# Kernel tuning notes

Measured on AMD Instinct MI355X. Metric: run time of the kernel, lower is better.

## Reference

```python
import jax, jax.numpy as jnp
import numpy as np

NUM_HEADS = 16
HEAD_DIM = 64
LN_EPS = 1e-5


def setup_inputs() -> dict:
    key = jax.random.key(0)
    k1, k2, k3, k4 = jax.random.split(key, 4)
    B, N, D = 4, 2048, NUM_HEADS * HEAD_DIM
    q = jax.random.normal(k1, (B, N, D), dtype=jnp.float32)
    k = jax.random.normal(k2, (B, N, D), dtype=jnp.float32)
    v = jax.random.normal(k3, (B, N, D), dtype=jnp.float32)
    W_out = jax.random.normal(k4, (D, D), dtype=jnp.float32) * (1.0 / np.sqrt(D))
    g = jnp.ones((D,), dtype=jnp.float32)
    return {"q": q, "k": k, "v": v, "W_out": W_out, "g": g}


def _split_heads(x):
    b, n, _ = x.shape
    return x.reshape(b, n, NUM_HEADS, HEAD_DIM).transpose(0, 2, 1, 3)  # b h n d


def reference(q, k, v, W_out, g):
    scale = HEAD_DIM ** -0.5
    qh = _split_heads(q) * scale          # [b,h,n,d]
    kh = _split_heads(k)                  # [b,h,m,d]
    vh = _split_heads(v)                  # [b,h,m,d]
    sim = jnp.einsum('bhnd,bhmd->bhnm', qh, kh)
    attn = jax.nn.softmax(sim.astype(jnp.float32), axis=-1)
    out = jnp.einsum('bhnm,bhmd->bhnd', attn, vh)
    b, h, n, d = out.shape
    out = out.transpose(0, 2, 1, 3).reshape(b, n, h * d)  # b n (h d)
    out = out @ W_out.T                   # Linear, no bias
    # LayerNorm (bias=False), biased variance
    mean = jnp.mean(out, axis=-1, keepdims=True)
    var = jnp.var(out, axis=-1, keepdims=True)
    return (out - mean) * jax.lax.rsqrt(var + LN_EPS) * g
```

## Files before the change

kernel.cpp:

```cpp
#include <hip/hip_runtime.h>
#include <hip/hip_bf16.h>


#define Bv 4
#define Nv 2048
#define Hv 16
#define DHv 64
#define Dv 1024
#define NT (Nv / 64)

#define KCONV_BLOCKS 4096
#define WCONV_BLOCKS 512
#define VT_BLOCKS 2048

#define L2E 1.44269504088896340736f

typedef __attribute__((ext_vector_type(8))) short short8;
typedef __attribute__((ext_vector_type(4))) float floatx4;

__device__ inline unsigned pack_bf2(float a, float b) {
    unsigned ua = __builtin_bit_cast(unsigned, a) + 0x8000u;
    unsigned ub = __builtin_bit_cast(unsigned, b) + 0x8000u;
    return __builtin_amdgcn_perm(ub, ua, 0x07060302u);
}

__device__ inline unsigned cvt_pk_bf16(float a, float b) {
    unsigned d;
    asm("v_cvt_pk_bf16_f32 %0, %1, %2" : "=v"(d) : "v"(a), "v"(b));
    return d;
}

__device__ inline unsigned bf2u_rte(float a, float b) {
    unsigned short ua = __builtin_bit_cast(unsigned short, __float2bfloat16(a));
    unsigned short ub = __builtin_bit_cast(unsigned short, __float2bfloat16(b));
    return (unsigned)ua | ((unsigned)ub << 16);
}

__device__ inline float max3f(float a, float b, float c) {
    return fmaxf(fmaxf(a, b), c);
}

__device__ inline void plswap16(unsigned &a, unsigned &b) {
    auto r = __builtin_amdgcn_permlane16_swap(a, b, false, false);
    a = r[0]; b = r[1];
}
__device__ inline void plswap32(unsigned &a, unsigned &b) {
    auto r = __builtin_amdgcn_permlane32_swap(a, b, false, false);
    a = r[0]; b = r[1];
}

__device__ inline float redq_max(float x) {
    unsigned a = __builtin_bit_cast(unsigned, x), b = a;
    plswap16(a, b);
    float m = fmaxf(__builtin_bit_cast(float, a), __builtin_bit_cast(float, b));
    unsigned c = __builtin_bit_cast(unsigned, m), d = c;
    plswap32(c, d);
    return fmaxf(__builtin_bit_cast(float, c), __builtin_bit_cast(float, d));
}

__global__ __launch_bounds__(256)
void prep_all(const float* __restrict__ K, __hip_bfloat16* __restrict__ Kb,
              const float* __restrict__ W, __hip_bfloat16* __restrict__ Wb,
              const float* __restrict__ v, __hip_bfloat16* __restrict__ vt) {
    __shared__ short T[64][76];
    int bid = blockIdx.x;
    if (bid < KCONV_BLOCKS + WCONV_BLOCKS) {
        const float* src;
        __hip_bfloat16* dst;
        if (bid < KCONV_BLOCKS) { src = K; dst = Kb; }
        else { src = W; dst = Wb; bid -= KCONV_BLOCKS; }
        int base = (bid * 256 + threadIdx.x) * 8;
        float4 f0 = *(const float4*)(src + base);
        float4 f1 = *(const float4*)(src + base + 4);
        uint4 u;
        u.x = pack_bf2(f0.x, f0.y);
        u.y = pack_bf2(f0.z, f0.w);
        u.z = pack_bf2(f1.x, f1.y);
        u.w = pack_bf2(f1.z, f1.w);
        *(uint4*)(dst + base) = u;
        return;
    }
    bid -= KCONV_BLOCKS + WCONV_BLOCKS;
    const int b = bid >> 9;
    const int rem = bid & 511;
    const int h = rem >> 5;
    const int n0 = (rem & 31) * 64;
    const int t = threadIdx.x;
    const int ir = t >> 4;
    const int d4 = (t & 15) * 4;
#pragma unroll
    for (int pass = 0; pass < 4; ++pass) {
        int n = pass * 16 + ir;
        float4 f = *(const float4*)(v + ((size_t)b * Nv + n0 + n) * Dv + h * DHv + d4);
        T[d4 + 0][n] = (short)(pack_bf2(f.x, f.x) & 0xffffu);
        T[d4 + 1][n] = (short)(pack_bf2(f.y, f.y) & 0xffffu);
        T[d4 + 2][n] = (short)(pack_bf2(f.z, f.z) & 0xffffu);
        T[d4 + 3][n] = (short)(pack_bf2(f.w, f.w) & 0xffffu);
    }
    __syncthreads();
    const int d = t >> 2, kg = (t & 3) * 16;
    unsigned u[8];
#pragma unroll
    for (int i = 0; i < 8; ++i)
        u[i] = (unsigned)(unsigned short)T[d][kg + 2 * i] |
               ((unsigned)(unsigned short)T[d][kg + 2 * i + 1] << 16);
    __hip_bfloat16* op = vt + ((size_t)(b * Hv + h) * DHv + d) * Nv + n0 + kg;
    *(uint4*)op = *(uint4*)&u[0];
    *(uint4*)(op + 8) = *(uint4*)&u[4];
}

__global__ __launch_bounds__(256, 8)
void attn_mfma_pre(const float* __restrict__ q,
                   const __hip_bfloat16* __restrict__ Kb,
                   const __hip_bfloat16* __restrict__ Vtb,
                   __hip_bfloat16* __restrict__ out) {
    __shared__ __align__(16) short Kt[2][64 * 64];
    __shared__ __align__(16) short Vt[2][64 * 64];

    const int t = threadIdx.x;
    const int wave = t >> 6, lane = t & 63;
    const int quad = lane >> 4, lr = lane & 15;
    const int b = blockIdx.z;
    const int lid2 = blockIdx.y * 32 + blockIdx.x;
    const int xcd = lid2 & 7, jj = lid2 >> 3;
    const int h = xcd * 2 + (jj >> 5);
    const int q0 = (jj & 31) * 64;
    const size_t qbh = ((size_t)b * Nv) * Dv + h * DHv;
    const __hip_bfloat16* kb = Kb + (size_t)b * Nv * Dv + h * DHv;
    const __hip_bfloat16* vtb = Vtb + (size_t)(b * Hv + h) * DHv * Nv;

    const int srow = lane >> 3;
    const int sg = lane & 7;
    auto stage = [&](int buf, int k0) {
#pragma unroll
        for (int c = 0; c < 2; ++c) {
            int blk = wave * 2 + c;
            int r = blk * 8 + srow;
            int g = sg ^ (r & 7);
            __builtin_amdgcn_global_load_lds(
                (const __attribute__((address_space(1))) unsigned*)(const void*)
                    (kb + (size_t)(k0 + r) * Dv + g * 8),
                (__attribute__((address_space(3))) unsigned*)(void*)&Kt[buf][blk * 512],
                16, 0, 0);
            __builtin_amdgcn_global_load_lds(
                (const __attribute__((address_space(1))) unsigned*)(const void*)
                    (vtb + (size_t)r * Nv + k0 + g * 8),
                (__attribute__((address_space(3))) unsigned*)(void*)&Vt[buf][blk * 512],
                16, 0, 0);
        }
    };

    stage(0, 0);

    short8 qfrag[2];
#pragma unroll
    for (int kh = 0; kh < 2; ++kh) {
        int row = q0 + wave * 16 + lr;
        const float* qp = q + qbh + (size_t)row * Dv + kh * 32 + quad * 8;
        float4 f0 = *(const float4*)qp;
        float4 f1 = *(const float4*)(qp + 4);
        int4 qi;
        qi.x = (int)pack_bf2(f0.x * 0.125f, f0.y * 0.125f);
        qi.y = (int)pack_bf2(f0.z * 0.125f, f0.w * 0.125f);
        qi.z = (int)pack_bf2(f1.x * 0.125f, f1.y * 0.125f);
        qi.w = (int)pack_bf2(f1.z * 0.125f, f1.w * 0.125f);
        qfrag[kh] = __builtin_bit_cast(short8, qi);
    }

    short8 ones_f;
    {
        unsigned w = (lr == 0) ? 0x3F803F80u : 0u;
        int4 oi = {(int)w, (int)w, (int)w, (int)w};
        ones_f = __builtin_bit_cast(short8, oi);
    }

    floatx4 o_acc[4] = {};
    floatx4 lsum = {};
    float mrow = -INFINITY;

#pragma unroll 2
    for (int it = 0; it < NT; ++it) {
        const int cur = it & 1;
        __syncthreads();
        if (it + 1 < NT) stage(1 - cur, (it + 1) * 64);

        floatx4 s_acc[4] = {};
        __builtin_amdgcn_s_setprio(1);
#pragma unroll
        for (int tt = 0; tt < 4; ++tt) {
            int row = tt * 16 + lr;
            short8 kf0 = *(const short8*)&Kt[cur][row * 64 + ((quad ^ (lr & 7)) << 3)];
            short8 kf1 = *(const short8*)&Kt[cur][row * 64 + (((4 + quad) ^ (lr & 7)) << 3)];
            s_acc[tt] = __builtin_amdgcn_mfma_f32_16x16x32_bf16(kf0, qfrag[0], s_acc[tt], 0, 0, 0);
            s_acc[tt] = __builtin_amdgcn_mfma_f32_16x16x32_bf16(kf1, qfrag[1], s_acc[tt], 0, 0, 0);
        }
        __builtin_amdgcn_s_setprio(0);

        float m0 = max3f(s_acc[0][0], s_acc[0][1], s_acc[0][2]);
        float m1 = max3f(s_acc[0][3], s_acc[1][0], s_acc[1][1]);
        float m2 = max3f(s_acc[1][2], s_acc[1][3], s_acc[2][0]);
        float m3 = max3f(s_acc[2][1], s_acc[2][2], s_acc[2][3]);
        float m4 = max3f(s_acc[3][0], s_acc[3][1], s_acc[3][2]);
        float m5 = max3f(m0, m1, s_acc[3][3]);
        float tmax = redq_max(max3f(m5, max3f(m2, m3, m4), -INFINITY));
        if (!__all(tmax <= mrow + 8.0f)) {
            float mnew = fmaxf(mrow, tmax);
            float alpha = __expf(mrow - mnew);
            mrow = mnew;
            lsum[0] *= alpha;
#pragma unroll
            for (int td = 0; td < 4; ++td)
#pragma unroll
                for (int r2 = 0; r2 < 4; ++r2) o_acc[td][r2] *= alpha;
        }
        float negmc = -(mrow * L2E);
        unsigned p2[8];
#pragma unroll
        for (int tt = 0; tt < 4; ++tt) {
            float p0 = __builtin_amdgcn_exp2f(__builtin_fmaf(s_acc[tt][0], L2E, negmc));
            float p1 = __builtin_amdgcn_exp2f(__builtin_fmaf(s_acc[tt][1], L2E, negmc));
            float pa = __builtin_amdgcn_exp2f(__builtin_fmaf(s_acc[tt][2], L2E, negmc));
            float pb = __builtin_amdgcn_exp2f(__builtin_fmaf(s_acc[tt][3], L2E, negmc));
            p2[tt * 2 + 0] = cvt_pk_bf16(p0, p1);
            p2[tt * 2 + 1] = cvt_pk_bf16(pa, pb);
        }

#pragma unroll
        for (int kh = 0; kh < 2; ++kh) {
            int tlo = 4 * kh, thi = 4 * kh + 2;
            unsigned a0 = p2[tlo + 0], b0 = p2[thi + 0];
            unsigned a1 = p2[tlo + 1], b1 = p2[thi + 1];
            plswap32(a0, b0);
            plswap16(a0, b0);
            plswap32(a1, b1);
            plswap16(a1, b1);
            int4 afi;
            afi.x = (int)a0;
            afi.y = (int)a1;
            afi.z = (int)b0;
            afi.w = (int)b1;
            short8 af = __builtin_bit_cast(short8, afi);
            __builtin_amdgcn_s_setprio(1);
#pragma unroll
            for (int td = 0; td < 4; ++td) {
                int d = td * 16 + lr;
                short8 vf = *(const short8*)&Vt[cur][d * 64 + (((kh * 4 + quad) ^ (lr & 7)) << 3)];
                o_acc[td] = __builtin_amdgcn_mfma_f32_16x16x32_bf16(vf, af, o_acc[td], 0, 0, 0);
            }
            lsum = __builtin_amdgcn_mfma_f32_16x16x32_bf16(ones_f, af, lsum, 0, 0, 0);
            __builtin_amdgcn_s_setprio(0);
        }
    }

    {
        float linv = __shfl(1.f / lsum[0], lr);
        int qrow = q0 + wave * 16 + lr;
        __hip_bfloat16* op = out + ((size_t)(b * Nv + qrow)) * Dv + h * DHv + quad * 4;
#pragma unroll
        for (int td = 0; td < 4; ++td) {
            uint2 w;
            w.x = bf2u_rte(o_acc[td][0] * linv, o_acc[td][1] * linv);
            w.y = bf2u_rte(o_acc[td][2] * linv, o_acc[td][3] * linv);
            *(uint2*)(op + td * 16) = w;
        }
    }
}

__global__ __launch_bounds__(256)
void proj_kernel(const __hip_bfloat16* __restrict__ A,
                 const __hip_bfloat16* __restrict__ Wb,
                 float* __restrict__ C) {
    __shared__ __align__(16) short As[2][128 * 64];
    __shared__ __align__(16) short Ws[2][128 * 64];

    const int t = threadIdx.x;
    const int wave = t >> 6, lane = t & 63;
    const int quad = lane >> 4, lr = lane & 15;
    const int wm = wave >> 1, wn = wave & 1;
    const int bx = blockIdx.x;
    const int xcd = bx & 7, j = bx >> 3;
    const int bm = (xcd * 8 + (j >> 3)) * 128;
    const int bn = (j & 7) * 128;

    floatx4 acc[4][4] = {};

    auto stage = [&](int buf, int k0) {
#pragma unroll
        for (int c = 0; c < 4; ++c) {
            const int blk = c * 4 + wave;
            const int r = blk * 8 + (lane >> 3);
            const int g = (lane & 7) ^ (r & 7);
            const __hip_bfloat16* ga = A + (size_t)(bm + r) * Dv + k0 + g * 8;
            const __hip_bfloat16* gw = Wb + (size_t)(bn + r) * Dv + k0 + g * 8;
            __builtin_amdgcn_global_load_lds(
                (const __attribute__((address_space(1))) unsigned int*)(const void*)ga,
                (__attribute__((address_space(3))) unsigned int*)(void*)&As[buf][blk * 512],
                16, 0, 0);
            __builtin_amdgcn_global_load_lds(
                (const __attribute__((address_space(1))) unsigned int*)(const void*)gw,
                (__attribute__((address_space(3))) unsigned int*)(void*)&Ws[buf][blk * 512],
                16, 0, 0);
        }
    };

    stage(0, 0);

#pragma unroll 2
    for (int it = 0; it < Dv / 64; ++it) {
        const int cur = it & 1;
        __syncthreads();
        if (it + 1 < Dv / 64) stage(1 - cur, (it + 1) * 64);

#pragma unroll
        for (int ks = 0; ks < 2; ++ks) {
            short8 af[4];
#pragma unroll
            for (int mb = 0; mb < 4; ++mb) {
                int row = wm * 64 + mb * 16 + lr;
                af[mb] = *(const short8*)&As[cur][row * 64 + (((ks * 4 + quad) ^ (lr & 7)) << 3)];
            }
#pragma unroll
            for (int nb = 0; nb < 4; ++nb) {
                int row = wn * 64 + nb * 16 + lr;
                short8 bf = *(const short8*)&Ws[cur][row * 64 + (((ks * 4 + quad) ^ (lr & 7)) << 3)];
#pragma unroll
                for (int mb = 0; mb < 4; ++mb)
                    acc[mb][nb] = __builtin_amdgcn_mfma_f32_16x16x32_bf16(af[mb], bf, acc[mb][nb], 0, 0, 0);
            }
        }
    }

#pragma unroll
    for (int mb = 0; mb < 4; ++mb)
#pragma unroll
        for (int nb = 0; nb < 4; ++nb) {
            int row = bm + wm * 64 + mb * 16 + quad * 4;
            int col = bn + wn * 64 + nb * 16 + lr;
#pragma unroll
            for (int r = 0; r < 4; ++r)
                C[(size_t)(row + r) * Dv + col] = acc[mb][nb][r];
        }
}

__global__ __launch_bounds__(256)
void ln_kernel(float* __restrict__ C,
               const float* __restrict__ g) {
    const int row = blockIdx.x;
    const int t = threadIdx.x;
    const int wave = t >> 6, lane = t & 63;

    float* rp = C + (size_t)row * Dv;
    float4 x = *(const float4*)(rp + t * 4);

    float s = x.x + x.y + x.z + x.w;
    float sq = x.x * x.x + x.y * x.y + x.z * x.z + x.w * x.w;
#pragma unroll
    for (int off = 32; off >= 1; off >>= 1) {
        s += __shfl_xor(s, off);
        sq += __shfl_xor(sq, off);
    }
    __shared__ float ss[4], ssq[4];
    if (lane == 0) { ss[wave] = s; ssq[wave] = sq; }
    __syncthreads();
    s = ss[0] + ss[1] + ss[2] + ss[3];
    sq = ssq[0] + ssq[1] + ssq[2] + ssq[3];

    const float rn = 1.f / (float)Dv;
    float mean = s * rn;
    float var = sq * rn - mean * mean;
    float inv = rsqrtf(var + 1e-5f);

    float4 gv = *(const float4*)(g + t * 4);

    float4 o;
    o.x = (x.x - mean) * inv * gv.x;
    o.y = (x.y - mean) * inv * gv.y;
    o.z = (x.z - mean) * inv * gv.z;
    o.w = (x.w - mean) * inv * gv.w;
    *(float4*)(rp + t * 4) = o;
}

extern "C" void kernel_launch(void* const* d_in, const int* in_sizes, int n_in,
                              void* d_out, int out_size, void* d_ws, size_t ws_size,
                              hipStream_t stream) {
    const float* q = (const float*)d_in[0];
    const float* k = (const float*)d_in[1];
    const float* v = (const float*)d_in[2];
    const float* W = (const float*)d_in[3];
    const float* g = (const float*)d_in[4];
    float* out = (float*)d_out;

    const size_t attnB = (size_t)Bv * Nv * Dv * 2;
    const size_t wbB = (size_t)Dv * Dv * 2;
    const size_t kbB = (size_t)Bv * Nv * Dv * 2;

    __hip_bfloat16* attn = (__hip_bfloat16*)d_ws;
    __hip_bfloat16* Wb = (__hip_bfloat16*)((char*)d_ws + attnB);
    __hip_bfloat16* Kb = (__hip_bfloat16*)((char*)d_ws + attnB + wbB);
    __hip_bfloat16* Vtb = (__hip_bfloat16*)((char*)d_ws + attnB + wbB + kbB);

    prep_all<<<KCONV_BLOCKS + WCONV_BLOCKS + VT_BLOCKS, 256, 0, stream>>>(k, Kb, W, Wb, v, Vtb);
    attn_mfma_pre<<<dim3(32, 16, Bv), 256, 0, stream>>>(q, Kb, Vtb, attn);
    proj_kernel<<<512, 256, 0, stream>>>(attn, Wb, out);
    ln_kernel<<<Bv * Nv, 256, 0, stream>>>(out, g);
}
```

Measured before the change: 272.0 us.

## Fuse output projection with LayerNorm in one full-row kernel

Replaces the tiled LDS-staged projection GEMM and separate LayerNorm kernel with a single kernel where each block computes 32 full rows of the output (8 waves each covering 128 columns). Row mean and variance are reduced from the accumulators via shuffles and shared memory, and the normalized result is written once. This removes the fp32 intermediate write and reread plus one launch. In exchange the GEMM drops LDS staging and double buffering, loading A and W fragments straight from global memory with poor coalescing and less reuse.

```diff
diff --git a/kernel.cpp b/kernel.cpp
--- a/kernel.cpp
+++ b/kernel.cpp
@@ -266,118 +266,101 @@
     }
 }
 
-__global__ __launch_bounds__(256)
-void proj_kernel(const __hip_bfloat16* __restrict__ A,
-                 const __hip_bfloat16* __restrict__ Wb,
-                 float* __restrict__ C) {
-    __shared__ __align__(16) short As[2][128 * 64];
-    __shared__ __align__(16) short Ws[2][128 * 64];
+__global__ __launch_bounds__(512)
+void proj_ln_kernel(const __hip_bfloat16* __restrict__ A,
+                    const __hip_bfloat16* __restrict__ Wb,
+                    const float* __restrict__ g,
+                    float* __restrict__ out) {
+    __shared__ float red[8][32][2];
+    __shared__ float mi[32][2];
 
     const int t = threadIdx.x;
     const int wave = t >> 6, lane = t & 63;
     const int quad = lane >> 4, lr = lane & 15;
-    const int wm = wave >> 1, wn = wave & 1;
-    const int bx = blockIdx.x;
-    const int xcd = bx & 7, j = bx >> 3;
-    const int bm = (xcd * 8 + (j >> 3)) * 128;
-    const int bn = (j & 7) * 128;
-
-    floatx4 acc[4][4] = {};
-
-    auto stage = [&](int buf, int k0) {
-#pragma unroll
-        for (int c = 0; c < 4; ++c) {
-            const int blk = c * 4 + wave;
-            const int r = blk * 8 + (lane >> 3);
-            const int g = (lane & 7) ^ (r & 7);
-            const __hip_bfloat16* ga = A + (size_t)(bm + r) * Dv + k0 + g * 8;
-            const __hip_bfloat16* gw = Wb + (size_t)(bn + r) * Dv + k0 + g * 8;
-            __builtin_amdgcn_global_load_lds(
-                (const __attribute__((address_space(1))) unsigned int*)(const void*)ga,
-                (__attribute__((address_space(3))) unsigned int*)(void*)&As[buf][blk * 512],
-                16, 0, 0);
-            __builtin_amdgcn_global_load_lds(
-                (const __attribute__((address_space(1))) unsigned int*)(const void*)gw,
-                (__attribute__((address_space(3))) unsigned int*)(void*)&Ws[buf][blk * 512],
-                16, 0, 0);
-        }
-    };
-
-    stage(0, 0);
-
-#pragma unroll 2
-    for (int it = 0; it < Dv / 64; ++it) {
-        const int cur = it & 1;
-        __syncthreads();
-        if (it + 1 < Dv / 64) stage(1 - cur, (it + 1) * 64);
-
-#pragma unroll
-        for (int ks = 0; ks < 2; ++ks) {
-            short8 af[4];
-#pragma unroll
-            for (int mb = 0; mb < 4; ++mb) {
-                int row = wm * 64 + mb * 16 + lr;
-                af[mb] = *(const short8*)&As[cur][row * 64 + (((ks * 4 + quad) ^ (lr & 7)) << 3)];
+    const int r0 = blockIdx.x * 32;
+    const int wc = wave * 128;
+
+    floatx4 acc[2][8] = {};
+
+    const __hip_bfloat16* arow0 = A + (size_t)(r0 + lr) * Dv + quad * 8;
+    const __hip_bfloat16* arow1 = arow0 + (size_t)16 * Dv;
+    const __hip_bfloat16* wrow = Wb + (size_t)(wc + lr) * Dv + quad * 8;
+
+    for (int k0 = 0; k0 < Dv; k0 += 32) {
+        short8 af0 = *(const short8*)(arow0 + k0);
+        short8 af1 = *(const short8*)(arow1 + k0);
+#pragma unroll
+        for (int ct = 0; ct < 8; ++ct) {
+            short8 wf = *(const short8*)(wrow + (size_t)ct * 16 * Dv + k0);
+            acc[0][ct] = __builtin_amdgcn_mfma_f32_16x16x32_bf16(af0, wf, acc[0][ct], 0, 0, 0);
+            acc[1][ct] = __builtin_amdgcn_mfma_f32_16x16x32_bf16(af1, wf, acc[1][ct], 0, 0, 0);
+        }
+    }
+
+    float s8[2][4], q8[2][4];
+#pragma unroll
+    for (int rt = 0; rt < 2; ++rt)
+#pragma unroll
+        for (int r = 0; r < 4; ++r) {
+            float s = 0.f, qq = 0.f;
+#pragma unroll
+            for (int ct = 0; ct < 8; ++ct) {
+                float v = acc[rt][ct][r];
+                s += v;
+                qq = __builtin_fmaf(v, v, qq);
             }
-#pragma unroll
-            for (int nb = 0; nb < 4; ++nb) {
-                int row = wn * 64 + nb * 16 + lr;
-                short8 bf = *(const short8*)&Ws[cur][row * 64 + (((ks * 4 + quad) ^ (lr & 7)) << 3)];
-#pragma unroll
-                for (int mb = 0; mb < 4; ++mb)
-                    acc[mb][nb] = __builtin_amdgcn_mfma_f32_16x16x32_bf16(af[mb], bf, acc[mb][nb], 0, 0, 0);
+            s8[rt][r] = s;
+            q8[rt][r] = qq;
+        }
+#pragma unroll
+    for (int m = 1; m <= 8; m <<= 1)
+#pragma unroll
+        for (int rt = 0; rt < 2; ++rt)
+#pragma unroll
+            for (int r = 0; r < 4; ++r) {
+                s8[rt][r] += __shfl_xor(s8[rt][r], m);
+                q8[rt][r] += __shfl_xor(q8[rt][r], m);
             }
-        }
-    }
-
-#pragma unroll
-    for (int mb = 0; mb < 4; ++mb)
-#pragma unroll
-        for (int nb = 0; nb < 4; ++nb) {
-            int row = bm + wm * 64 + mb * 16 + quad * 4;
-            int col = bn + wn * 64 + nb * 16 + lr;
-#pragma unroll
-            for (int r = 0; r < 4; ++r)
-                C[(size_t)(row + r) * Dv + col] = acc[mb][nb][r];
-        }
-}
-
-__global__ __launch_bounds__(256)
-void ln_kernel(float* __restrict__ C,
-               const float* __restrict__ g) {
-    const int row = blockIdx.x;
-    const int t = threadIdx.x;
-    const int wave = t >> 6, lane = t & 63;
-
-    float* rp = C + (size_t)row * Dv;
-    float4 x = *(const float4*)(rp + t * 4);
-
-    float s = x.x + x.y + x.z + x.w;
-    float sq = x.x * x.x + x.y * x.y + x.z * x.z + x.w * x.w;
-#pragma unroll
-    for (int off = 32; off >= 1; off >>= 1) {
-        s += __shfl_xor(s, off);
-        sq += __shfl_xor(sq, off);
-    }
-    __shared__ float ss[4], ssq[4];
-    if (lane == 0) { ss[wave] = s; ssq[wave] = sq; }
+    if (lr == 0) {
+#pragma unroll
+        for (int rt = 0; rt < 2; ++rt)
+#pragma unroll
+            for (int r = 0; r < 4; ++r) {
+                int row = rt * 16 + quad * 4 + r;
+                red[wave][row][0] = s8[rt][r];
+                red[wave][row][1] = q8[rt][r];
+            }
+    }
     __syncthreads();
-    s = ss[0] + ss[1] + ss[2] + ss[3];
-    sq = ssq[0] + ssq[1] + ssq[2] + ssq[3];
-
-    const float rn = 1.f / (float)Dv;
-    float mean = s * rn;
-    float var = sq * rn - mean * mean;
-    float inv = rsqrtf(var + 1e-5f);
-
-    float4 gv = *(const float4*)(g + t * 4);
-
-    float4 o;
-    o.x = (x.x - mean) * inv * gv.x;
-    o.y = (x.y - mean) * inv * gv.y;
-    o.z = (x.z - mean) * inv * gv.z;
-    o.w = (x.w - mean) * inv * gv.w;
-    *(float4*)(rp + t * 4) = o;
+    if (t < 32) {
+        float s = 0.f, qq = 0.f;
+#pragma unroll
+        for (int w = 0; w < 8; ++w) {
+            s += red[w][t][0];
+            qq += red[w][t][1];
+        }
+        const float rn = 1.f / (float)Dv;
+        float mean = s * rn;
+        float var = qq * rn - mean * mean;
+        mi[t][0] = mean;
+        mi[t][1] = rsqrtf(var + 1e-5f);
+    }
+    __syncthreads();
+
+    float gv[8];
+#pragma unroll
+    for (int ct = 0; ct < 8; ++ct) gv[ct] = g[wc + ct * 16 + lr];
+#pragma unroll
+    for (int rt = 0; rt < 2; ++rt)
+#pragma unroll
+        for (int r = 0; r < 4; ++r) {
+            int row = rt * 16 + quad * 4 + r;
+            float mean = mi[row][0], inv = mi[row][1];
+            float* op = out + (size_t)(r0 + row) * Dv + wc + lr;
+#pragma unroll
+            for (int ct = 0; ct < 8; ++ct)
+                op[ct * 16] = (acc[rt][ct][r] - mean) * inv * gv[ct];
+        }
 }
 
 extern "C" void kernel_launch(void* const* d_in, const int* in_sizes, int n_in,
@@ -401,6 +384,5 @@
 
     prep_all<<<KCONV_BLOCKS + WCONV_BLOCKS + VT_BLOCKS, 256, 0, stream>>>(k, Kb, W, Wb, v, Vtb);
     attn_mfma_pre<<<dim3(32, 16, Bv), 256, 0, stream>>>(q, Kb, Vtb, attn);
-    proj_kernel<<<512, 256, 0, stream>>>(attn, Wb, out);
-    ln_kernel<<<Bv * Nv, 256, 0, stream>>>(out, g);
-}
+    proj_ln_kernel<<<(Bv * Nv) / 32, 512, 0, stream>>>(attn, Wb, g, out);
+}
```

After: 323.9 us. +19.1%, slower.
